# Kernel optimization log

Hardware: AMD Instinct MI355X
Metric: run time of the kernel (lower is better)

Reference implementation:

```python
import jax, jax.numpy as jnp
import numpy as np
import math

DIM = 512
HEADS = 8
HEAD_DIM = DIM // HEADS
WINDOW = 16
HIDDEN = 4 * DIM
SCALE = HEAD_DIM ** (-0.5)


def _best_hw(n):
    r = int(math.sqrt(n))
    best = (1, n)
    min_gap = n - 1
    for h in range(1, r + 1):
        if n % h == 0:
            w = n // h
            if abs(w - h) < min_gap:
                min_gap = abs(w - h)
                best = (h, w)
    return best


def _pad_to_window(x, w):
    # x: [B,C,H,W]
    B, C, H, W = x.shape
    ph = (-H) % w
    pw = (-W) % w
    if ph or pw:
        x = jnp.pad(x, ((0, 0), (0, 0), (0, ph), (0, pw)))
    return x, (ph, pw)


def _window_partition(x, w):
    # [B,C,Hp,Wp] -> [B*nW, w*w, C]
    B, C, Hp, Wp = x.shape
    x = x.reshape(B, C, Hp // w, w, Wp // w, w)
    x = jnp.transpose(x, (0, 2, 4, 3, 5, 1))  # [B,nWh,nWw,w,w,C]
    return x.reshape(-1, w * w, C), (Hp, Wp, Hp // w, Wp // w)


def _window_reverse(windows, w, meta):
    Hp, Wp, nWh, nWw = meta
    B = windows.shape[0] // (nWh * nWw)
    C = windows.shape[-1]
    x = windows.reshape(B, nWh, nWw, w, w, C)
    x = jnp.transpose(x, (0, 5, 1, 3, 2, 4))
    return x.reshape(B, C, Hp, Wp)


def _branch(src, oth, Wq, bq, Wk, bk, Wv, bv, Wo, bo, W1, b1, W2, b2):
    # src acts as query grid; oth is resized onto src's grid (cross attention)
    B, N, C = src.shape
    Hs, Ws = _best_hw(N)
    src_map = jnp.transpose(src, (0, 2, 1)).reshape(B, C, Hs, Ws)
    M = oth.shape[1]
    Ho, Wo_sp = _best_hw(M)
    oth_map = jnp.transpose(oth, (0, 2, 1)).reshape(B, C, Ho, Wo_sp)
    # bilinear resize, half-pixel centers (== torch align_corners=False, no antialias)
    oth_rs = jax.image.resize(oth_map, (B, C, Hs, Ws), method='bilinear', antialias=False)

    src_pad, (ph, pw) = _pad_to_window(src_map, WINDOW)
    oth_pad, _ = _pad_to_window(oth_rs, WINDOW)
    src_win, meta = _window_partition(src_pad, WINDOW)   # [Bn,T,C]
    oth_win, _ = _window_partition(oth_pad, WINDOW)

    q = src_win @ Wq + bq
    k = oth_win @ Wk + bk
    v = src_win @ Wv + bv
    Bn, T, _ = q.shape
    q = q.reshape(Bn, T, HEADS, HEAD_DIM)
    k = k.reshape(Bn, T, HEADS, HEAD_DIM)
    v = v.reshape(Bn, T, HEADS, HEAD_DIM)
    attn = jnp.einsum('bthd,bshd->bhts', q, k) * SCALE
    attn = jax.nn.softmax(attn, axis=-1)  # dropout is identity in eval
    out = jnp.einsum('bhts,bshd->bthd', attn, v).reshape(Bn, T, C)
    out = out @ Wo + bo

    out_map = _window_reverse(out, WINDOW, meta)
    Hp, Wp = out_map.shape[-2:]
    if ph or pw:
        out_map = out_map[:, :, :Hp - ph, :Wp - pw]
    tokens = jnp.transpose(out_map.reshape(B, C, -1), (0, 2, 1)) + src
    # MLP (GELU exact, dropout identity)
    h = jax.nn.gelu(tokens @ W1 + b1, approximate=False)
    tokens = (h @ W2 + b2) + tokens
    return tokens


def setup_inputs() -> dict:
    key = jax.random.key(0)
    ks = jax.random.split(key, 16)
    s = 0.02
    return {
        'x': jax.random.normal(ks[0], (8, 4096, DIM), jnp.float32),
        'y': jax.random.normal(ks[1], (8, 1024, DIM), jnp.float32),
        'Wq': jax.random.normal(ks[2], (DIM, DIM), jnp.float32) * s,
        'bq': jnp.zeros((DIM,), jnp.float32),
        'Wk': jax.random.normal(ks[3], (DIM, DIM), jnp.float32) * s,
        'bk': jnp.zeros((DIM,), jnp.float32),
        'Wv': jax.random.normal(ks[4], (DIM, DIM), jnp.float32) * s,
        'bv': jnp.zeros((DIM,), jnp.float32),
        'Wo': jax.random.normal(ks[5], (DIM, DIM), jnp.float32) * s,
        'bo': jnp.zeros((DIM,), jnp.float32),
        'W1': jax.random.normal(ks[6], (DIM, HIDDEN), jnp.float32) * s,
        'b1': jnp.zeros((HIDDEN,), jnp.float32),
        'W2': jax.random.normal(ks[7], (HIDDEN, DIM), jnp.float32) * s,
        'b2': jnp.zeros((DIM,), jnp.float32),
    }


def reference(x, y, Wq, bq, Wk, bk, Wv, bv, Wo, bo, W1, b1, W2, b2):
    out_x = _branch(x, y, Wq, bq, Wk, bk, Wv, bv, Wo, bo, W1, b1, W2, b2)
    out_y = _branch(y, x, Wq, bq, Wk, bk, Wv, bv, Wo, bo, W1, b1, W2, b2)
    return jnp.concatenate([out_x, out_y], axis=1)  # [B, N+M, C]
```

## Files before the change

kernel.cpp:

```cpp
#include <hip/hip_runtime.h>
#include <hip/hip_bf16.h>
#include <math.h>

typedef __attribute__((ext_vector_type(8))) __bf16 bf8_t;
typedef __attribute__((ext_vector_type(4))) float f4_t;
typedef __attribute__((ext_vector_type(4))) int   i4_t;

#define XTOK 32768
#define NTOK 40960
#define DIMC 512

__device__ __forceinline__ void gload_lds16(const __bf16* g, __bf16* l) {
  __builtin_amdgcn_global_load_lds((const __attribute__((address_space(1))) void*)g,
                                   (__attribute__((address_space(3))) void*)l, 16, 0, 0);
}
__device__ __forceinline__ float bflo(unsigned u) { union { unsigned x; float f; } c; c.x = u << 16; return c.f; }
__device__ __forceinline__ float bfhi(unsigned u) { union { unsigned x; float f; } c; c.x = u & 0xffff0000u; return c.f; }

__device__ __forceinline__ float gelu_fast(float v) {
  float u = v * 0.70710678118654752f;
  float a = fabsf(u);
  float t = __builtin_amdgcn_rcpf(1.0f + 0.3275911f * a);
  float e = __builtin_amdgcn_exp2f(-a * a * 1.4426950408889634f);
  float poly = t * (0.254829592f + t * (-0.284496736f + t * (1.421413741f +
               t * (-1.453152027f + t * 1.061405429f))));
  float erfa = 1.0f - poly * e;
  float erfu = (u < 0.0f) ? -erfa : erfa;
  return 0.5f * v * (1.0f + erfu);
}

__global__ void transpose_all(const float* __restrict__ Wq, const float* __restrict__ Wv,
                              const float* __restrict__ Wk, const float* __restrict__ Wo,
                              const float* __restrict__ W1, const float* __restrict__ W2,
                              __bf16* __restrict__ WqvT, __bf16* __restrict__ WkT,
                              __bf16* __restrict__ WoT, __bf16* __restrict__ W1T,
                              __bf16* __restrict__ W2T) {
  __shared__ float t[32][33];
  int b = blockIdx.x;
  const float* W; __bf16* WT; int K, N, tb;
  if (b < 256)       { W = Wq; WT = WqvT;                       K = 512;  N = 512;  tb = b; }
  else if (b < 512)  { W = Wv; WT = WqvT + (size_t)512 * 512;   K = 512;  N = 512;  tb = b - 256; }
  else if (b < 768)  { W = Wk; WT = WkT;                        K = 512;  N = 512;  tb = b - 512; }
  else if (b < 1024) { W = Wo; WT = WoT;                        K = 512;  N = 512;  tb = b - 768; }
  else if (b < 2048) { W = W1; WT = W1T;                        K = 512;  N = 2048; tb = b - 1024; }
  else               { W = W2; WT = W2T;                        K = 2048; N = 512;  tb = b - 2048; }
  int ntn = N >> 5;
  int bk = (tb / ntn) * 32, bn = (tb - (tb / ntn) * ntn) * 32;
  int tx = threadIdx.x & 31, ty = threadIdx.x >> 5;
#pragma unroll
  for (int i = 0; i < 4; ++i)
    t[ty + i * 8][tx] = W[(size_t)(bk + ty + i * 8) * N + bn + tx];
  __syncthreads();
#pragma unroll
  for (int i = 0; i < 4; ++i)
    WT[(size_t)(bn + ty + i * 8) * K + bk + tx] = (__bf16)t[tx][ty + i * 8];
}

__global__ void pack_tokens(const float* __restrict__ x, const float* __restrict__ y,
                            __bf16* __restrict__ Asrc, __bf16* __restrict__ Aoth,
                            int* __restrict__ srcoff, int* __restrict__ outoff) {
  int g = blockIdx.x;
  int t = threadIdx.x;
  int b, h, w; int soff, ooff; bool isx = (g < XTOK);
  if (isx) {
    b = g >> 12;
    int w5 = g & 4095;
    int widx = w5 >> 8, tt = w5 & 255;
    int wh = widx >> 2, ww = widx & 3;
    h = wh * 16 + (tt >> 4); w = ww * 16 + (tt & 15);
    int n = h * 64 + w;
    soff = (b * 4096 + n) * 512;
    ooff = (b * 5120 + n) * 512;
  } else {
    int gy = g - XTOK;
    b = gy >> 10;
    int w5 = gy & 1023;
    int widx = w5 >> 8, tt = w5 & 255;
    int wh = widx >> 1, ww = widx & 1;
    h = wh * 16 + (tt >> 4); w = ww * 16 + (tt & 15);
    int n = h * 32 + w;
    soff = (b * 1024 + n) * 512;
    ooff = (b * 5120 + 4096 + n) * 512;
  }
  if (t == 0) { srcoff[g] = soff; outoff[g] = ooff; }
  const float* sp = (isx ? x : y) + (size_t)soff + t * 2;
  float2 sv = *(const float2*)sp;
  size_t gb = (size_t)g * 512 + t * 2;
  Asrc[gb]     = (__bf16)sv.x;
  Asrc[gb + 1] = (__bf16)sv.y;

  float o0, o1;
  if (isx) {
    int h0, h1, w0i, w1i; float fh0, fh1, fw0, fw1;
    if (h & 1) { h0 = h >> 1; h1 = (h0 + 1 < 31) ? h0 + 1 : 31; fh0 = 0.75f; fh1 = 0.25f; }
    else       { h1 = h >> 1; h0 = (h1 - 1 > 0) ? h1 - 1 : 0;   fh0 = 0.25f; fh1 = 0.75f; }
    if (w & 1) { w0i = w >> 1; w1i = (w0i + 1 < 31) ? w0i + 1 : 31; fw0 = 0.75f; fw1 = 0.25f; }
    else       { w1i = w >> 1; w0i = (w1i - 1 > 0) ? w1i - 1 : 0;   fw0 = 0.25f; fw1 = 0.75f; }
    const float* yb = y + (size_t)b * 1024 * 512 + t * 2;
    float2 v00 = *(const float2*)(yb + (h0 * 32 + w0i) * 512);
    float2 v01 = *(const float2*)(yb + (h0 * 32 + w1i) * 512);
    float2 v10 = *(const float2*)(yb + (h1 * 32 + w0i) * 512);
    float2 v11 = *(const float2*)(yb + (h1 * 32 + w1i) * 512);
    o0 = fh0 * (fw0 * v00.x + fw1 * v01.x) + fh1 * (fw0 * v10.x + fw1 * v11.x);
    o1 = fh0 * (fw0 * v00.y + fw1 * v01.y) + fh1 * (fw0 * v10.y + fw1 * v11.y);
  } else {
    const float* xb = x + (size_t)b * 4096 * 512 + t * 2;
    float2 v00 = *(const float2*)(xb + ((2 * h) * 64 + 2 * w) * 512);
    float2 v01 = *(const float2*)(xb + ((2 * h) * 64 + 2 * w + 1) * 512);
    float2 v10 = *(const float2*)(xb + ((2 * h + 1) * 64 + 2 * w) * 512);
    float2 v11 = *(const float2*)(xb + ((2 * h + 1) * 64 + 2 * w + 1) * 512);
    o0 = 0.25f * (v00.x + v01.x + v10.x + v11.x);
    o1 = 0.25f * (v00.y + v01.y + v10.y + v11.y);
  }
  Aoth[gb]     = (__bf16)o0;
  Aoth[gb + 1] = (__bf16)o1;
}

template<int EPI>
__global__ __launch_bounds__(256, 2)
void gemm_bt(const __bf16* __restrict__ A, const __bf16* __restrict__ BT,
             const float* __restrict__ bias, const float* __restrict__ bias2,
             int K, int nbn, int row0,
             __bf16* __restrict__ outb, __bf16* __restrict__ outb2,
             const float* __restrict__ resx, const float* __restrict__ resy,
             const int* __restrict__ srcoff, const int* __restrict__ outoff,
             const __bf16* __restrict__ toksr, float* __restrict__ dout,
             const __bf16* __restrict__ A2, const __bf16* __restrict__ BT2,
             const float* __restrict__ bias3, __bf16* __restrict__ outb3) {
  const int N = nbn * 128;
  __shared__ __align__(16) __bf16 smem[17408];
  int nwg = gridDim.x;
  int qq = nwg >> 3, rr = nwg & 7;
  int xcd = blockIdx.x & 7, base = blockIdx.x >> 3;
  int wg = (xcd < rr ? xcd * (qq + 1) : rr * (qq + 1) + (xcd - rr) * qq) + base;

  bool isK = false;
  int bm, bn;
  const __bf16* Ap = A;
  const __bf16* Bp = BT;
  if (EPI == 5) {
    isK = (wg >= row0);
    if (isK) { int w2 = wg - row0; bm = w2 >> 2; bn = w2 & 3; Ap = A2; Bp = BT2; }
    else     { bm = wg >> 3; bn = wg & 7; }
  } else {
    bm = wg / nbn; bn = wg - bm * nbn;
  }
  int m0 = bm * 128, n0 = bn * 128;

  int tid = threadIdx.x, lane = tid & 63, wid = tid >> 6;
  int wr = wid >> 1, wc = wid & 1;
  int ln15 = lane & 15, kq = lane >> 4;

  f4_t acc[4][4];
#pragma unroll
  for (int m = 0; m < 4; ++m)
#pragma unroll
    for (int n = 0; n < 4; ++n) acc[m][n] = f4_t{0.f, 0.f, 0.f, 0.f};

  int offA[4], offB[4];
#pragma unroll
  for (int m = 0; m < 4; ++m) {
    int row = wr * 64 + m * 16 + ln15;
    offA[m] = row * 32 + ((kq ^ (row & 3) ^ ((row >> 2) & 3)) << 3);
  }
#pragma unroll
  for (int n = 0; n < 4; ++n) {
    int row = wc * 64 + n * 16 + ln15;
    offB[n] = 4096 + row * 32 + ((kq ^ (row & 3) ^ ((row >> 2) & 3)) << 3);
  }
  int srow[2], scol[2], sdst[2];
#pragma unroll
  for (int j = 0; j < 2; ++j) {
    int ci = (wid * 2 + j) * 64 + lane;
    int row = ci >> 2;
    srow[j] = row;
    scol[j] = ((ci & 3) ^ (row & 3) ^ ((row >> 2) & 3)) * 8;
    sdst[j] = (wid * 2 + j) * 512;
  }

  auto stage = [&](int slotbase, int kt) {
    int k0 = kt << 5;
#pragma unroll
    for (int j = 0; j < 2; ++j) {
      gload_lds16(Ap + (size_t)(m0 + srow[j]) * K + k0 + scol[j], &smem[slotbase + sdst[j]]);
      gload_lds16(Bp + (size_t)(n0 + srow[j]) * K + k0 + scol[j], &smem[slotbase + 4096 + sdst[j]]);
    }
  };

#define GEMM_HALF(SLOTBASE)                                                       \
  do {                                                                            \
    bf8_t av[4], bv[4];                                                           \
    _Pragma("unroll")                                                             \
    for (int m = 0; m < 4; ++m) av[m] = *(const bf8_t*)&smem[(SLOTBASE) + offA[m]]; \
    _Pragma("unroll")                                                             \
    for (int n = 0; n < 4; ++n) bv[n] = *(const bf8_t*)&smem[(SLOTBASE) + offB[n]]; \
    __builtin_amdgcn_s_setprio(1);                                                \
    _Pragma("unroll")                                                             \
    for (int m = 0; m < 4; ++m) {                                                 \
      _Pragma("unroll")                                                           \
      for (int n = 0; n < 4; ++n)                                                 \
        acc[m][n] = __builtin_amdgcn_mfma_f32_16x16x32_bf16(av[m], bv[n], acc[m][n], 0, 0, 0); \
    }                                                                             \
    __builtin_amdgcn_s_setprio(0);                                                \
  } while (0)

  int nt = K >> 5;
  stage(0, 0);
  __syncthreads();
  for (int t = 0; t < nt; t += 2) {
    stage(8192, t + 1);
    GEMM_HALF(0);
    __syncthreads();
    if (t + 2 < nt) stage(0, t + 2);
    GEMM_HALF(8192);
    __syncthreads();
  }
#undef GEMM_HALF

  bool hi = (EPI == 5) && !isK && (n0 >= 512);
  const float* bptr = (EPI == 5 && isK) ? bias3 : (hi ? bias2 : bias);
  int nbase = hi ? n0 - 512 : n0;
  float bs[4];
#pragma unroll
  for (int n = 0; n < 4; ++n) bs[n] = bptr[nbase + wc * 64 + n * 16 + ln15];

#pragma unroll
  for (int m = 0; m < 4; ++m) {
    int lr2 = m0 + wr * 64 + m * 16 + kq * 4;
#pragma unroll
    for (int r = 0; r < 4; ++r) {
      int grow = row0 + lr2 + r;
      const float* rptr = nullptr; int so = 0;
      if (EPI == 1) { so = srcoff[grow]; rptr = (grow < XTOK) ? resx : resy; }
#pragma unroll
      for (int n = 0; n < 4; ++n) {
        int gcol = nbase + wc * 64 + n * 16 + ln15;
        float v = acc[m][n][r] + bs[n];
        if (EPI == 1) v += rptr[(size_t)so + gcol];
        if (EPI == 2) v = gelu_fast(v);
        if (EPI == 3) v += (float)toksr[(size_t)grow * DIMC + gcol];
        acc[m][n][r] = v;
      }
    }
  }

  if (EPI != 3) {
#pragma unroll
    for (int m = 0; m < 4; ++m)
#pragma unroll
      for (int r = 0; r < 4; ++r)
#pragma unroll
        for (int n = 0; n < 4; ++n)
          smem[(wr * 64 + m * 16 + kq * 4 + r) * 136 + wc * 64 + n * 16 + ln15] = (__bf16)acc[m][n][r];
    __syncthreads();
    __bf16* ob = (EPI == 5) ? (isK ? outb3 : (hi ? outb2 : outb)) : outb;
    int ldn = (EPI == 2) ? N : 512;
    int gc0 = (EPI == 2) ? n0 : nbase;
#pragma unroll
    for (int it = 0; it < 8; ++it) {
      int cid = it * 256 + tid;
      int row = cid >> 4, c = cid & 15;
      i4_t v = *(const i4_t*)&smem[row * 136 + c * 8];
      *(i4_t*)&ob[(size_t)(m0 + row) * ldn + gc0 + c * 8] = v;
    }
  } else {
    float* stf = (float*)smem;
#pragma unroll
    for (int h = 0; h < 2; ++h) {
      __syncthreads();
      if (wc == h) {
#pragma unroll
        for (int m = 0; m < 4; ++m)
#pragma unroll
          for (int r = 0; r < 4; ++r)
#pragma unroll
            for (int n = 0; n < 4; ++n)
              stf[(wr * 64 + m * 16 + kq * 4 + r) * 68 + n * 16 + ln15] = acc[m][n][r];
      }
      __syncthreads();
#pragma unroll
      for (int it = 0; it < 8; ++it) {
        int cid = it * 256 + tid;
        int row = cid >> 4, c = cid & 15;
        f4_t v = *(const f4_t*)&stf[row * 68 + c * 4];
        int oo = outoff[row0 + m0 + row];
        *(f4_t*)&dout[(size_t)oo + n0 + h * 64 + c * 4] = v;
      }
    }
  }
}

__global__ __launch_bounds__(512, 2)
void attn_kernel(const __bf16* __restrict__ Qb, const __bf16* __restrict__ Kb,
                 const __bf16* __restrict__ Vb, __bf16* __restrict__ AOb) {
  __shared__ __align__(16) __bf16 smem[32768];
  __bf16* Kl = smem;
  __bf16* Vt = smem + 16384;
  int tid = threadIdx.x, lane = tid & 63, wid = tid >> 6;
  int l15 = lane & 15, kq = lane >> 4;
  int win = blockIdx.x >> 3, head = blockIdx.x & 7;
  size_t wtok = (size_t)win * 256;
  int hc = head * 64;

#pragma unroll
  for (int it = 0; it < 4; ++it) {
    int i = (wid * 4 + it) * 64 + lane;
    int s = i >> 3, cp = i & 7, c = cp ^ (s & 7);
    gload_lds16(Kb + (wtok + s) * 512 + hc + c * 8, &Kl[(size_t)((wid * 4 + it) * 64) * 8]);
  }
#pragma unroll
  for (int it = 0; it < 4; ++it) {
    int j = tid + it * 512;
    int dc = j & 7, s = j >> 3;
    i4_t v = *(const i4_t*)(Vb + (wtok + s) * 512 + hc + dc * 8);
    const __bf16* ve = (const __bf16*)&v;
#pragma unroll
    for (int jj = 0; jj < 8; ++jj) {
      int d = dc * 8 + jj;
      int sc = (s >> 3) ^ (((d >> 3) ^ d) & 7);
      Vt[d * 256 + (sc << 3) + (s & 7)] = ve[jj];
    }
  }
  __syncthreads();

  const float CLOG2E = 0.18033688011112043f;
  f4_t oacc[2][4];
  float rinvq[2];
  int sl0 = ((kq & 1) << 5) + l15;
  int sl1 = sl0 + 16;
  bool hiT = (kq & 2) != 0;

#pragma unroll
  for (int qt = 0; qt < 2; ++qt) {
    int qbase = wid * 32 + qt * 16;
    bf8_t qf[2];
#pragma unroll
    for (int k2 = 0; k2 < 2; ++k2)
      qf[k2] = *(const bf8_t*)(Qb + (wtok + qbase + l15) * 512 + hc + k2 * 32 + kq * 8);

    uint2 ps[16];
    float mx = -3.0e38f;
    __builtin_amdgcn_s_setprio(1);
#pragma unroll
    for (int st = 0; st < 16; ++st) {
      f4_t z = {0.f, 0.f, 0.f, 0.f};
      int s = st * 16 + l15;
#pragma unroll
      for (int k2 = 0; k2 < 2; ++k2) {
        int c = (k2 * 4 + kq) ^ (s & 7);
        bf8_t kf = *(const bf8_t*)&Kl[(s * 8 + c) * 8];
        z = __builtin_amdgcn_mfma_f32_16x16x32_bf16(kf, qf[k2], z, 0, 0, 0);
      }
      z *= CLOG2E;
      mx = fmaxf(mx, fmaxf(fmaxf(z[0], z[1]), fmaxf(z[2], z[3])));
      union { __bf16 b[4]; uint2 u; } pk;
#pragma unroll
      for (int r = 0; r < 4; ++r) pk.b[r] = (__bf16)z[r];
      ps[st] = pk.u;
    }
    __builtin_amdgcn_s_setprio(0);
    mx = fmaxf(mx, __shfl_xor(mx, 16, 64));
    mx = fmaxf(mx, __shfl_xor(mx, 32, 64));

    float L = 0.f;
#pragma unroll
    for (int st = 0; st < 16; ++st) {
      uint2 u = ps[st];
      float p0 = __builtin_amdgcn_exp2f(bflo(u.x) - mx);
      float p1 = __builtin_amdgcn_exp2f(bfhi(u.x) - mx);
      float p2 = __builtin_amdgcn_exp2f(bflo(u.y) - mx);
      float p3 = __builtin_amdgcn_exp2f(bfhi(u.y) - mx);
      L += (p0 + p1) + (p2 + p3);
      union { __bf16 b[4]; uint2 u; } pk;
      pk.b[0] = (__bf16)p0; pk.b[1] = (__bf16)p1; pk.b[2] = (__bf16)p2; pk.b[3] = (__bf16)p3;
      ps[st] = pk.u;
    }
    L += __shfl_xor(L, 16, 64);
    L += __shfl_xor(L, 32, 64);
    rinvq[qt] = __builtin_amdgcn_rcpf(L);

#pragma unroll
    for (int dn = 0; dn < 4; ++dn) oacc[qt][dn] = f4_t{0.f, 0.f, 0.f, 0.f};
    __builtin_amdgcn_s_setprio(1);
#pragma unroll
    for (int c = 0; c < 8; ++c) {
      uint2 t0 = ps[2 * c], t1 = ps[2 * c + 1];
      int a00x = __shfl((int)t0.x, sl0, 64), a00y = __shfl((int)t0.y, sl0, 64);
      int a01x = __shfl((int)t0.x, sl1, 64), a01y = __shfl((int)t0.y, sl1, 64);
      int a10x = __shfl((int)t1.x, sl0, 64), a10y = __shfl((int)t1.y, sl0, 64);
      int a11x = __shfl((int)t1.x, sl1, 64), a11y = __shfl((int)t1.y, sl1, 64);
      union { int u[4]; bf8_t v; } fr;
      fr.u[0] = hiT ? a10x : a00x;
      fr.u[1] = hiT ? a10y : a00y;
      fr.u[2] = hiT ? a11x : a01x;
      fr.u[3] = hiT ? a11y : a01y;
#pragma unroll
      for (int dn = 0; dn < 4; ++dn) {
        int d = dn * 16 + l15;
        int sc = (4 * c + kq) ^ (((d >> 3) ^ d) & 7);
        bf8_t vf = *(const bf8_t*)&Vt[d * 256 + (sc << 3)];
        oacc[qt][dn] = __builtin_amdgcn_mfma_f32_16x16x32_bf16(fr.v, vf, oacc[qt][dn], 0, 0, 0);
      }
    }
    __builtin_amdgcn_s_setprio(0);
  }

  __syncthreads();
  __bf16* Ko = smem + wid * 2304;
#pragma unroll
  for (int qt = 0; qt < 2; ++qt)
#pragma unroll
    for (int dn = 0; dn < 4; ++dn)
#pragma unroll
      for (int r = 0; r < 4; ++r)
        Ko[(qt * 16 + kq * 4 + r) * 72 + dn * 16 + l15] = (__bf16)(oacc[qt][dn][r] * rinvq[qt]);
#pragma unroll
  for (int it = 0; it < 4; ++it) {
    int lr = it * 8 + (lane >> 3), cb = (lane & 7) * 8;
    i4_t v = *(const i4_t*)&Ko[lr * 72 + cb];
    *(i4_t*)&AOb[(wtok + wid * 32 + lr) * 512 + hc + cb] = v;
  }
}

extern "C" void kernel_launch(void* const* d_in, const int* in_sizes, int n_in,
                              void* d_out, int out_size, void* d_ws, size_t ws_size,
                              hipStream_t stream) {
  const float* x  = (const float*)d_in[0];
  const float* y  = (const float*)d_in[1];
  const float* Wq = (const float*)d_in[2];
  const float* bq = (const float*)d_in[3];
  const float* Wk = (const float*)d_in[4];
  const float* bk = (const float*)d_in[5];
  const float* Wv = (const float*)d_in[6];
  const float* bv = (const float*)d_in[7];
  const float* Wo = (const float*)d_in[8];
  const float* bo = (const float*)d_in[9];
  const float* W1 = (const float*)d_in[10];
  const float* b1 = (const float*)d_in[11];
  const float* W2 = (const float*)d_in[12];
  const float* b2 = (const float*)d_in[13];

  char* ws = (char*)d_ws;
  size_t off = 0;
  auto carve = [&](size_t bytes) -> void* {
    void* p = ws + off;
    off += (bytes + 255) & ~(size_t)255;
    return p;
  };
  __bf16* WqvT = (__bf16*)carve((size_t)1024 * 512 * 2);
  __bf16* WkT  = (__bf16*)carve((size_t)512 * 512 * 2);
  __bf16* WoT  = (__bf16*)carve((size_t)512 * 512 * 2);
  __bf16* W1T  = (__bf16*)carve((size_t)2048 * 512 * 2);
  __bf16* W2T  = (__bf16*)carve((size_t)512 * 2048 * 2);
  int* srcoff = (int*)carve((size_t)NTOK * 4);
  int* outoff = (int*)carve((size_t)NTOK * 4);
  __bf16* Asrc = (__bf16*)carve((size_t)NTOK * 512 * 2);
  __bf16* Aoth = (__bf16*)carve((size_t)NTOK * 512 * 2);
  __bf16* Qb   = (__bf16*)carve((size_t)NTOK * 512 * 2);
  __bf16* Kb   = (__bf16*)carve((size_t)NTOK * 512 * 2);
  __bf16* Vb   = (__bf16*)carve((size_t)NTOK * 512 * 2);
  int nc = 1;
  while (nc < 4 && off + (size_t)(NTOK / nc) * 2048 * 2 > ws_size) nc *= 2;
  int rows = NTOK / nc;
  __bf16* Hb = (__bf16*)carve((size_t)rows * 2048 * 2);
  __bf16* AOb   = Asrc;
  __bf16* toksb = Aoth;
  float*  dout  = (float*)d_out;

  transpose_all<<<3072, 256, 0, stream>>>(Wq, Wv, Wk, Wo, W1, W2, WqvT, WkT, WoT, W1T, W2T);

  pack_tokens<<<NTOK, 256, 0, stream>>>(x, y, Asrc, Aoth, srcoff, outoff);

  gemm_bt<5><<<NTOK / 128 * 12, 256, 0, stream>>>(Asrc, WqvT, bq, bv, 512, 8, NTOK / 128 * 8,
      Qb, Vb, nullptr, nullptr, nullptr, nullptr, nullptr, nullptr, Aoth, WkT, bk, Kb);

  attn_kernel<<<160 * 8, 512, 0, stream>>>(Qb, Kb, Vb, AOb);

  gemm_bt<1><<<NTOK / 128 * 4, 256, 0, stream>>>(AOb, WoT, bo, nullptr, 512, 4, 0, toksb, nullptr,
      x, y, srcoff, nullptr, nullptr, nullptr, nullptr, nullptr, nullptr, nullptr);

  for (int c = 0; c < nc; ++c) {
    int r0 = c * rows;
    gemm_bt<2><<<rows / 128 * 16, 256, 0, stream>>>(toksb + (size_t)r0 * 512, W1T, b1, nullptr,
        512, 16, r0, Hb, nullptr, nullptr, nullptr, nullptr, nullptr, nullptr, nullptr,
        nullptr, nullptr, nullptr, nullptr);
    gemm_bt<3><<<rows / 128 * 4, 256, 0, stream>>>(Hb, W2T, b2, nullptr, 2048, 4, r0,
        nullptr, nullptr, nullptr, nullptr, nullptr, outoff, toksb, dout,
        nullptr, nullptr, nullptr, nullptr);
  }
}
```

Before: 519.5 us.

## Fuse weight transpose into token packing and read residual from packed bf16 tokens

Merges the weight-transpose kernel into the token-packing kernel as extra blocks, removing one launch. The out-projection epilogue now adds the residual from the already-packed bf16 source tokens instead of gathering fp32 x/y through a srcoff table, which cuts scattered fp32 reads and the srcoff array. The workspace plan changes: attention output gets its own buffer, the hidden activation reuses the Q buffer, and the FFN is fixed at two chunks. The residual is now rounded to bf16, a small accuracy loss. The fixed chunking assumes the Q buffer is large enough for the hidden chunk, which it is at these sizes.

```diff
diff --git a/kernel.cpp b/kernel.cpp
--- a/kernel.cpp
+++ b/kernel.cpp
@@ -29,45 +29,46 @@
   return 0.5f * v * (1.0f + erfu);
 }
 
-__global__ void transpose_all(const float* __restrict__ Wq, const float* __restrict__ Wv,
-                              const float* __restrict__ Wk, const float* __restrict__ Wo,
-                              const float* __restrict__ W1, const float* __restrict__ W2,
-                              __bf16* __restrict__ WqvT, __bf16* __restrict__ WkT,
-                              __bf16* __restrict__ WoT, __bf16* __restrict__ W1T,
-                              __bf16* __restrict__ W2T) {
-  __shared__ float t[32][33];
-  int b = blockIdx.x;
-  const float* W; __bf16* WT; int K, N, tb;
-  if (b < 256)       { W = Wq; WT = WqvT;                       K = 512;  N = 512;  tb = b; }
-  else if (b < 512)  { W = Wv; WT = WqvT + (size_t)512 * 512;   K = 512;  N = 512;  tb = b - 256; }
-  else if (b < 768)  { W = Wk; WT = WkT;                        K = 512;  N = 512;  tb = b - 512; }
-  else if (b < 1024) { W = Wo; WT = WoT;                        K = 512;  N = 512;  tb = b - 768; }
-  else if (b < 2048) { W = W1; WT = W1T;                        K = 512;  N = 2048; tb = b - 1024; }
-  else               { W = W2; WT = W2T;                        K = 2048; N = 512;  tb = b - 2048; }
-  int ntn = N >> 5;
-  int bk = (tb / ntn) * 32, bn = (tb - (tb / ntn) * ntn) * 32;
-  int tx = threadIdx.x & 31, ty = threadIdx.x >> 5;
-#pragma unroll
-  for (int i = 0; i < 4; ++i)
-    t[ty + i * 8][tx] = W[(size_t)(bk + ty + i * 8) * N + bn + tx];
-  __syncthreads();
-#pragma unroll
-  for (int i = 0; i < 4; ++i)
-    WT[(size_t)(bn + ty + i * 8) * K + bk + tx] = (__bf16)t[tx][ty + i * 8];
-}
-
-__global__ void pack_tokens(const float* __restrict__ x, const float* __restrict__ y,
-                            __bf16* __restrict__ Asrc, __bf16* __restrict__ Aoth,
-                            int* __restrict__ srcoff, int* __restrict__ outoff) {
+__global__ void pack_and_transpose(const float* __restrict__ x, const float* __restrict__ y,
+                                   __bf16* __restrict__ Asrc, __bf16* __restrict__ Aoth,
+                                   int* __restrict__ outoff,
+                                   const float* __restrict__ Wq, const float* __restrict__ Wv,
+                                   const float* __restrict__ Wk, const float* __restrict__ Wo,
+                                   const float* __restrict__ W1, const float* __restrict__ W2,
+                                   __bf16* __restrict__ WqvT, __bf16* __restrict__ WkT,
+                                   __bf16* __restrict__ WoT, __bf16* __restrict__ W1T,
+                                   __bf16* __restrict__ W2T) {
+  __shared__ float tt32[32][33];
   int g = blockIdx.x;
   int t = threadIdx.x;
+  if (g >= NTOK) {
+    int b = g - NTOK;
+    const float* W; __bf16* WT; int K, N, tb;
+    if (b < 256)       { W = Wq; WT = WqvT;                       K = 512;  N = 512;  tb = b; }
+    else if (b < 512)  { W = Wv; WT = WqvT + (size_t)512 * 512;   K = 512;  N = 512;  tb = b - 256; }
+    else if (b < 768)  { W = Wk; WT = WkT;                        K = 512;  N = 512;  tb = b - 512; }
+    else if (b < 1024) { W = Wo; WT = WoT;                        K = 512;  N = 512;  tb = b - 768; }
+    else if (b < 2048) { W = W1; WT = W1T;                        K = 512;  N = 2048; tb = b - 1024; }
+    else               { W = W2; WT = W2T;                        K = 2048; N = 512;  tb = b - 2048; }
+    int ntn = N >> 5;
+    int bk = (tb / ntn) * 32, bn = (tb - (tb / ntn) * ntn) * 32;
+    int tx = t & 31, ty = t >> 5;
+#pragma unroll
+    for (int i = 0; i < 4; ++i)
+      tt32[ty + i * 8][tx] = W[(size_t)(bk + ty + i * 8) * N + bn + tx];
+    __syncthreads();
+#pragma unroll
+    for (int i = 0; i < 4; ++i)
+      WT[(size_t)(bn + ty + i * 8) * K + bk + tx] = (__bf16)tt32[tx][ty + i * 8];
+    return;
+  }
   int b, h, w; int soff, ooff; bool isx = (g < XTOK);
   if (isx) {
     b = g >> 12;
     int w5 = g & 4095;
-    int widx = w5 >> 8, tt = w5 & 255;
+    int widx = w5 >> 8, tk = w5 & 255;
     int wh = widx >> 2, ww = widx & 3;
-    h = wh * 16 + (tt >> 4); w = ww * 16 + (tt & 15);
+    h = wh * 16 + (tk >> 4); w = ww * 16 + (tk & 15);
     int n = h * 64 + w;
     soff = (b * 4096 + n) * 512;
     ooff = (b * 5120 + n) * 512;
@@ -75,14 +76,14 @@
     int gy = g - XTOK;
     b = gy >> 10;
     int w5 = gy & 1023;
-    int widx = w5 >> 8, tt = w5 & 255;
+    int widx = w5 >> 8, tk = w5 & 255;
     int wh = widx >> 1, ww = widx & 1;
-    h = wh * 16 + (tt >> 4); w = ww * 16 + (tt & 15);
+    h = wh * 16 + (tk >> 4); w = ww * 16 + (tk & 15);
     int n = h * 32 + w;
     soff = (b * 1024 + n) * 512;
     ooff = (b * 5120 + 4096 + n) * 512;
   }
-  if (t == 0) { srcoff[g] = soff; outoff[g] = ooff; }
+  if (t == 0) { outoff[g] = ooff; }
   const float* sp = (isx ? x : y) + (size_t)soff + t * 2;
   float2 sv = *(const float2*)sp;
   size_t gb = (size_t)g * 512 + t * 2;
@@ -122,8 +123,7 @@
              const float* __restrict__ bias, const float* __restrict__ bias2,
              int K, int nbn, int row0,
              __bf16* __restrict__ outb, __bf16* __restrict__ outb2,
-             const float* __restrict__ resx, const float* __restrict__ resy,
-             const int* __restrict__ srcoff, const int* __restrict__ outoff,
+             const int* __restrict__ outoff,
              const __bf16* __restrict__ toksr, float* __restrict__ dout,
              const __bf16* __restrict__ A2, const __bf16* __restrict__ BT2,
              const float* __restrict__ bias3, __bf16* __restrict__ outb3) {
@@ -230,15 +230,12 @@
 #pragma unroll
     for (int r = 0; r < 4; ++r) {
       int grow = row0 + lr2 + r;
-      const float* rptr = nullptr; int so = 0;
-      if (EPI == 1) { so = srcoff[grow]; rptr = (grow < XTOK) ? resx : resy; }
 #pragma unroll
       for (int n = 0; n < 4; ++n) {
         int gcol = nbase + wc * 64 + n * 16 + ln15;
         float v = acc[m][n][r] + bs[n];
-        if (EPI == 1) v += rptr[(size_t)so + gcol];
+        if (EPI == 1 || EPI == 3) v += (float)toksr[(size_t)grow * DIMC + gcol];
         if (EPI == 2) v = gelu_fast(v);
-        if (EPI == 3) v += (float)toksr[(size_t)grow * DIMC + gcol];
         acc[m][n][r] = v;
       }
     }
@@ -452,40 +449,36 @@
   __bf16* WoT  = (__bf16*)carve((size_t)512 * 512 * 2);
   __bf16* W1T  = (__bf16*)carve((size_t)2048 * 512 * 2);
   __bf16* W2T  = (__bf16*)carve((size_t)512 * 2048 * 2);
-  int* srcoff = (int*)carve((size_t)NTOK * 4);
   int* outoff = (int*)carve((size_t)NTOK * 4);
   __bf16* Asrc = (__bf16*)carve((size_t)NTOK * 512 * 2);
   __bf16* Aoth = (__bf16*)carve((size_t)NTOK * 512 * 2);
   __bf16* Qb   = (__bf16*)carve((size_t)NTOK * 512 * 2);
   __bf16* Kb   = (__bf16*)carve((size_t)NTOK * 512 * 2);
   __bf16* Vb   = (__bf16*)carve((size_t)NTOK * 512 * 2);
-  int nc = 1;
-  while (nc < 4 && off + (size_t)(NTOK / nc) * 2048 * 2 > ws_size) nc *= 2;
-  int rows = NTOK / nc;
-  __bf16* Hb = (__bf16*)carve((size_t)rows * 2048 * 2);
-  __bf16* AOb   = Asrc;
+  __bf16* AOb  = (__bf16*)carve((size_t)NTOK * 512 * 2);
   __bf16* toksb = Aoth;
+  __bf16* Hb    = Qb;
   float*  dout  = (float*)d_out;
-
-  transpose_all<<<3072, 256, 0, stream>>>(Wq, Wv, Wk, Wo, W1, W2, WqvT, WkT, WoT, W1T, W2T);
-
-  pack_tokens<<<NTOK, 256, 0, stream>>>(x, y, Asrc, Aoth, srcoff, outoff);
+  const int nc = 2, rows = NTOK / 2;
+
+  pack_and_transpose<<<NTOK + 3072, 256, 0, stream>>>(x, y, Asrc, Aoth, outoff,
+      Wq, Wv, Wk, Wo, W1, W2, WqvT, WkT, WoT, W1T, W2T);
 
   gemm_bt<5><<<NTOK / 128 * 12, 256, 0, stream>>>(Asrc, WqvT, bq, bv, 512, 8, NTOK / 128 * 8,
-      Qb, Vb, nullptr, nullptr, nullptr, nullptr, nullptr, nullptr, Aoth, WkT, bk, Kb);
+      Qb, Vb, nullptr, nullptr, nullptr, Aoth, WkT, bk, Kb);
 
   attn_kernel<<<160 * 8, 512, 0, stream>>>(Qb, Kb, Vb, AOb);
 
-  gemm_bt<1><<<NTOK / 128 * 4, 256, 0, stream>>>(AOb, WoT, bo, nullptr, 512, 4, 0, toksb, nullptr,
-      x, y, srcoff, nullptr, nullptr, nullptr, nullptr, nullptr, nullptr, nullptr);
+  gemm_bt<1><<<NTOK / 128 * 4, 256, 0, stream>>>(AOb, WoT, bo, nullptr, 512, 4, 0,
+      toksb, nullptr, nullptr, Asrc, nullptr, nullptr, nullptr, nullptr, nullptr);
 
   for (int c = 0; c < nc; ++c) {
     int r0 = c * rows;
     gemm_bt<2><<<rows / 128 * 16, 256, 0, stream>>>(toksb + (size_t)r0 * 512, W1T, b1, nullptr,
-        512, 16, r0, Hb, nullptr, nullptr, nullptr, nullptr, nullptr, nullptr, nullptr,
+        512, 16, r0, Hb, nullptr, nullptr, nullptr, nullptr,
         nullptr, nullptr, nullptr, nullptr);
     gemm_bt<3><<<rows / 128 * 4, 256, 0, stream>>>(Hb, W2T, b2, nullptr, 2048, 4, r0,
-        nullptr, nullptr, nullptr, nullptr, nullptr, outoff, toksb, dout,
+        nullptr, nullptr, outoff, toksb, dout,
         nullptr, nullptr, nullptr, nullptr);
   }
 }
```

Result: no change. 510.8 us (-1.7%).
